# Optimization experiments

Hardware: AMD Instinct MI355X
Metric: run time of the kernel (lower is better)

Reference implementation:

```python
import jax, jax.numpy as jnp
import numpy as np
from jax import lax

N = 200000
CIN = 64
COUT = 128
K = 27  # 3^3 kernel offsets
EPS = 1e-5


def _make_rulebook(key, n, k):
    ki, km = jax.random.split(key)
    idx = jax.random.randint(ki, (k, n), 0, n, dtype=jnp.int32)
    keep = jax.random.uniform(km, (k, n)) < 0.5
    idx = jnp.where(keep, idx, -1)
    # center offset is always the voxel itself (submanifold conv)
    idx = idx.at[k // 2].set(jnp.arange(n, dtype=jnp.int32))
    return idx


def setup_inputs() -> dict:
    key = jax.random.key(0)
    ks = jax.random.split(key, 8)
    feats = jax.random.normal(ks[0], (N, CIN), dtype=jnp.float32)
    nbr1 = _make_rulebook(ks[1], N, K)
    nbr2 = _make_rulebook(ks[2], N, K)
    W1 = jax.random.normal(ks[3], (K, CIN, COUT), dtype=jnp.float32) * 0.05
    W2 = jax.random.normal(ks[4], (K, COUT, COUT), dtype=jnp.float32) * 0.05
    Wd = jax.random.normal(ks[5], (CIN, COUT), dtype=jnp.float32) * 0.05
    g1 = jnp.ones((COUT,), jnp.float32); b1 = jnp.zeros((COUT,), jnp.float32)
    g2 = jnp.ones((COUT,), jnp.float32); b2 = jnp.zeros((COUT,), jnp.float32)
    gd = jnp.ones((COUT,), jnp.float32); bd = jnp.zeros((COUT,), jnp.float32)
    return dict(feats=feats, nbr1=nbr1, nbr2=nbr2, W1=W1, W2=W2, Wd=Wd,
                g1=g1, b1=b1, g2=g2, b2=b2, gd=gd, bd=bd)


def sparse_conv(feats, W, nbr):
    """Rulebook sparse conv: gather neighbors per offset, GEMM, accumulate.
    feats: [N, Cin]; W: [K, Cin, Cout]; nbr: [K, N] int (-1 = missing)."""
    n = feats.shape[0]
    acc0 = jnp.zeros((n, W.shape[-1]), feats.dtype)

    def body(acc, xs):
        idx, Wk = xs  # [N], [Cin, Cout]
        valid = (idx >= 0).astype(feats.dtype)[:, None]
        g = feats[jnp.clip(idx, 0)] * valid  # masked gather [N, Cin]
        return acc + g @ Wk, None

    out, _ = lax.scan(body, acc0, (nbr, W))
    return out


def batchnorm(x, gamma, beta):
    mean = jnp.mean(x, axis=0)
    var = jnp.var(x, axis=0)
    return (x - mean) * lax.rsqrt(var + EPS) * gamma + beta


def reference(feats, nbr1, nbr2, W1, W2, Wd, g1, b1, g2, b2, gd, bd):
    h = sparse_conv(feats, W1, nbr1)
    h = jax.nn.relu(batchnorm(h, g1, b1))
    h = sparse_conv(h, W2, nbr2)
    h = batchnorm(h, g2, b2)
    skip = batchnorm(feats @ Wd, gd, bd)  # 1x1 conv downsample (Cin != Cout)
    return jax.nn.relu(h + skip)
```

## Files before the change

kernel.cpp:

```cpp
#include <hip/hip_runtime.h>
#include <stdint.h>

#define KOFF 27
#define CIN 64
#define COUT 128
#define EPS 1e-5f

using frag_ab = __attribute__((ext_vector_type(8))) short;
using frag_cd = __attribute__((ext_vector_type(4))) float;

__device__ __forceinline__ float bf2f(unsigned short u) {
  union { unsigned int i; float f; } x; x.i = ((unsigned int)u) << 16; return x.f;
}
__device__ __forceinline__ unsigned short f2bf(float f) {
  union { float f; unsigned int i; } x; x.f = f;
  unsigned int u = x.i;
  u += 0x7fffu + ((u >> 16) & 1u);
  return (unsigned short)(u >> 16);
}

__device__ __forceinline__ void gld16(const void* gptr, void* lptr) {
  __builtin_amdgcn_global_load_lds(
      (const __attribute__((address_space(1))) unsigned int*)gptr,
      (__attribute__((address_space(3))) unsigned int*)lptr, 16, 0, 0);
}

template <int CI, bool GATHER, bool OF32>
__global__ __launch_bounds__(256, 3) void conv_kernel(
    const unsigned short* __restrict__ X, const int* __restrict__ nbr,
    const unsigned short* __restrict__ Wt, void* __restrict__ Yv,
    const unsigned short* __restrict__ zpage, float* __restrict__ sums,
    int n, int koff) {
  constexpr int NC = CI / 32;
  __shared__ unsigned short Alds[3][128 * 32];
  __shared__ unsigned short Blds[3][128 * 32];

  const int tid = threadIdx.x;
  const int lane = tid & 63;
  const int wave = tid >> 6;
  const int row0 = blockIdx.x * 128;
  const int wrow = (wave >> 1) * 64;
  const int wcol = (wave & 1) * 64;
  const int m = lane & 15;
  const int q = lane >> 4;
  const int srow0 = wave * 16 + (lane >> 2);
  const int sl = lane & 3;

  frag_cd acc[4][4];
#pragma unroll
  for (int i = 0; i < 4; ++i)
#pragma unroll
    for (int j = 0; j < 4; ++j) acc[i][j] = (frag_cd){0.f, 0.f, 0.f, 0.f};

  int idxc[2], idxn[2];
  auto load_idx = [&](int ko, int (&dst)[2]) {
#pragma unroll
    for (int i = 0; i < 2; ++i) {
      const int grow = row0 + srow0 + i * 64;
      int v = -1;
      if (grow < n) v = GATHER ? nbr[(size_t)ko * n + grow] : grow;
      dst[i] = v;
    }
  };
  auto stage = [&](int buf, int ko, int kc, const int (&idx)[2]) {
#pragma unroll
    for (int i = 0; i < 2; ++i) {
      const int row = srow0 + i * 64;
      const int g = sl ^ ((row >> 1) & 3);
      const unsigned short* ga =
          (idx[i] >= 0) ? X + (size_t)idx[i] * CI + kc * 32 + g * 8 : zpage;
      gld16(ga, &Alds[buf][(i * 64 + wave * 16) * 32]);
      const unsigned short* gb =
          Wt + (size_t)ko * (128 * CI) + (size_t)row * CI + kc * 32 + g * 8;
      gld16(gb, &Blds[buf][(i * 64 + wave * 16) * 32]);
    }
  };
  auto do_mfma = [&](int buf) {
    frag_ab a[4], b[4];
#pragma unroll
    for (int i = 0; i < 4; ++i) {
      const int row = wrow + 16 * i + m;
      a[i] = *(const frag_ab*)(&Alds[buf][row * 32 + (q ^ ((row >> 1) & 3)) * 8]);
    }
#pragma unroll
    for (int j = 0; j < 4; ++j) {
      const int row = wcol + 16 * j + m;
      b[j] = *(const frag_ab*)(&Blds[buf][row * 32 + (q ^ ((row >> 1) & 3)) * 8]);
    }
#pragma unroll
    for (int i = 0; i < 4; ++i)
#pragma unroll
      for (int j = 0; j < 4; ++j)
        acc[i][j] = __builtin_amdgcn_mfma_f32_16x16x32_bf16(a[i], b[j],
                                                            acc[i][j], 0, 0, 0);
  };

  const int T = koff * NC;
  load_idx(0, idxc);
  stage(0, 0, 0, idxc);
  stage(1, 0, 1, idxc);
  if (koff > 1) load_idx(1, idxn);

  int bufc = 0;
  for (int t = 0; t < T - 1; ++t) {
    asm volatile("s_waitcnt vmcnt(4)" ::: "memory");
    __builtin_amdgcn_s_barrier();
    const int s = t + 2;
    if (s < T) {
      const int kos = s / NC;
      const int kcs = s & (NC - 1);
      if (kcs == 0) {
        idxc[0] = idxn[0];
        idxc[1] = idxn[1];
        if (kos + 1 < koff) load_idx(kos + 1, idxn);
      }
      int bufs = bufc + 2; if (bufs >= 3) bufs -= 3;
      stage(bufs, kos, kcs, idxc);
    }
    do_mfma(bufc);
    if (++bufc == 3) bufc = 0;
  }
  asm volatile("s_waitcnt vmcnt(0)" ::: "memory");
  __builtin_amdgcn_s_barrier();
  do_mfma(bufc);

#pragma unroll
  for (int j = 0; j < 4; ++j) {
    float s = 0.f, qq = 0.f;
#pragma unroll
    for (int i = 0; i < 4; ++i)
#pragma unroll
      for (int r = 0; r < 4; ++r) {
        float v = acc[i][j][r];
        s += v; qq += v * v;
      }
    s += __shfl_xor(s, 16); s += __shfl_xor(s, 32);
    qq += __shfl_xor(qq, 16); qq += __shfl_xor(qq, 32);
    if (lane < 16) {
      const int col = wcol + 16 * j + lane;
      atomicAdd(&sums[col], s);
      atomicAdd(&sums[COUT + col], qq);
    }
  }

#pragma unroll
  for (int i = 0; i < 4; ++i) {
#pragma unroll
    for (int r = 0; r < 4; ++r) {
      const int grow = row0 + wrow + 16 * i + q * 4 + r;
      if (grow < n) {
#pragma unroll
        for (int j = 0; j < 4; ++j) {
          const int gcol = wcol + 16 * j + m;
          if (OF32)
            ((float*)Yv)[(size_t)grow * COUT + gcol] = acc[i][j][r];
          else
            ((unsigned short*)Yv)[(size_t)grow * COUT + gcol] = f2bf(acc[i][j][r]);
        }
      }
    }
  }
}

__global__ void convert_kernel(const float* __restrict__ src,
                               unsigned short* __restrict__ dst, int total8) {
  int gid = blockIdx.x * 256 + threadIdx.x;
  if (gid >= total8) return;
  const float* s = src + (size_t)gid * 8;
  float4 lo = *(const float4*)s;
  float4 hi = *(const float4*)(s + 4);
  uint4 r;
  r.x = (unsigned)f2bf(lo.x) | ((unsigned)f2bf(lo.y) << 16);
  r.y = (unsigned)f2bf(lo.z) | ((unsigned)f2bf(lo.w) << 16);
  r.z = (unsigned)f2bf(hi.x) | ((unsigned)f2bf(hi.y) << 16);
  r.w = (unsigned)f2bf(hi.z) | ((unsigned)f2bf(hi.w) << 16);
  *(uint4*)(dst + (size_t)gid * 8) = r;
}

__global__ void transpose_w(const float* __restrict__ src,
                            unsigned short* __restrict__ dst, int kk, int ci,
                            int co) {
  int gid = blockIdx.x * blockDim.x + threadIdx.x;
  int total = kk * ci * co;
  if (gid >= total) return;
  int per = ci * co;
  int k = gid / per;
  int rem = gid - k * per;
  int o = rem / ci;
  int i = rem - o * ci;
  dst[gid] = f2bf(src[(size_t)k * per + (size_t)i * co + o]);
}

__global__ void finalize_kernel(const float* __restrict__ sums,
                                const float* __restrict__ gamma,
                                const float* __restrict__ beta,
                                float* __restrict__ scale,
                                float* __restrict__ shift, int n) {
  int c = threadIdx.x;
  float inv_n = 1.f / (float)n;
  float mean = sums[c] * inv_n;
  float var = sums[COUT + c] * inv_n - mean * mean;
  float sc = gamma[c] * rsqrtf(var + EPS);
  scale[c] = sc;
  shift[c] = beta[c] - mean * sc;
}

__global__ void norm_relu_kernel(unsigned short* __restrict__ x,
                                 const float* __restrict__ scale,
                                 const float* __restrict__ shift, int total8) {
  int gid = blockIdx.x * 256 + threadIdx.x;
  if (gid >= total8) return;
  size_t i = (size_t)gid * 8;
  int c0 = (int)(i & 127);
  uint4 v = *(const uint4*)(x + i);
  unsigned int w[4] = {v.x, v.y, v.z, v.w};
  unsigned int wo[4];
#pragma unroll
  for (int e = 0; e < 4; ++e) {
    int c = c0 + 2 * e;
    float f0 = bf2f((unsigned short)(w[e] & 0xffffu));
    float f1 = bf2f((unsigned short)(w[e] >> 16));
    f0 = fmaxf(f0 * scale[c] + shift[c], 0.f);
    f1 = fmaxf(f1 * scale[c + 1] + shift[c + 1], 0.f);
    wo[e] = (unsigned int)f2bf(f0) | ((unsigned int)f2bf(f1) << 16);
  }
  *(uint4*)(x + i) = make_uint4(wo[0], wo[1], wo[2], wo[3]);
}

__global__ void final_kernel(float* __restrict__ h2,
                             const unsigned short* __restrict__ s,
                             const float* __restrict__ scale2,
                             const float* __restrict__ shift2,
                             const float* __restrict__ scaled,
                             const float* __restrict__ shiftd, int total4) {
  int gid = blockIdx.x * 256 + threadIdx.x;
  if (gid >= total4) return;
  size_t i = (size_t)gid * 4;
  int c = (int)(i & 127);
  float4 a = *(const float4*)(h2 + i);
  uint2 sv = *(const uint2*)(s + i);
  float b0 = bf2f((unsigned short)(sv.x & 0xffffu));
  float b1 = bf2f((unsigned short)(sv.x >> 16));
  float b2 = bf2f((unsigned short)(sv.y & 0xffffu));
  float b3 = bf2f((unsigned short)(sv.y >> 16));
  float4 o;
  o.x = fmaxf(a.x * scale2[c] + shift2[c] + b0 * scaled[c] + shiftd[c], 0.f);
  o.y = fmaxf(a.y * scale2[c + 1] + shift2[c + 1] + b1 * scaled[c + 1] + shiftd[c + 1], 0.f);
  o.z = fmaxf(a.z * scale2[c + 2] + shift2[c + 2] + b2 * scaled[c + 2] + shiftd[c + 2], 0.f);
  o.w = fmaxf(a.w * scale2[c + 3] + shift2[c + 3] + b3 * scaled[c + 3] + shiftd[c + 3], 0.f);
  *(float4*)(h2 + i) = o;
}

extern "C" void kernel_launch(void* const* d_in, const int* in_sizes, int n_in,
                              void* d_out, int out_size, void* d_ws,
                              size_t ws_size, hipStream_t stream) {
  (void)n_in; (void)out_size; (void)ws_size;
  const float* feats = (const float*)d_in[0];
  const int* nbr1 = (const int*)d_in[1];
  const int* nbr2 = (const int*)d_in[2];
  const float* W1 = (const float*)d_in[3];
  const float* W2 = (const float*)d_in[4];
  const float* Wd = (const float*)d_in[5];
  const float* g1 = (const float*)d_in[6];
  const float* b1 = (const float*)d_in[7];
  const float* g2 = (const float*)d_in[8];
  const float* b2 = (const float*)d_in[9];
  const float* gd = (const float*)d_in[10];
  const float* bd = (const float*)d_in[11];

  const int n = in_sizes[0] / CIN;

  char* ws = (char*)d_ws;
  unsigned short* Wt1 = (unsigned short*)(ws);
  unsigned short* Wt2 = (unsigned short*)(ws + 442368);
  unsigned short* Wdt = (unsigned short*)(ws + 1327104);
  unsigned short* h1 = (unsigned short*)(ws + 1343488);
  unsigned short* sX = (unsigned short*)(ws + 52543488);
  float* sums1 = (float*)(ws + 103743488);
  float* sums2 = sums1 + 2 * COUT;
  float* sumsd = sums1 + 4 * COUT;
  float* scale1 = sums1 + 6 * COUT;
  float* shift1 = scale1 + COUT;
  float* scale2 = scale1 + 2 * COUT;
  float* shift2 = scale1 + 3 * COUT;
  float* scaled = scale1 + 4 * COUT;
  float* shiftd = scale1 + 5 * COUT;
  unsigned short* zpage = (unsigned short*)(ws + 103743488 + 8192);

  float* h2 = (float*)d_out;
  unsigned short* featsb = (unsigned short*)((char*)d_out + 76800000);

  hipMemsetAsync(sums1, 0, 8192 + 256, stream);

  transpose_w<<<(KOFF * CIN * COUT + 255) / 256, 256, 0, stream>>>(W1, Wt1, KOFF, CIN, COUT);
  transpose_w<<<(KOFF * COUT * COUT + 255) / 256, 256, 0, stream>>>(W2, Wt2, KOFF, COUT, COUT);
  transpose_w<<<(CIN * COUT + 255) / 256, 256, 0, stream>>>(Wd, Wdt, 1, CIN, COUT);

  const int f8 = n * CIN / 8;
  convert_kernel<<<(f8 + 255) / 256, 256, 0, stream>>>(feats, featsb, f8);

  const int mblocks = (n + 127) / 128;
  conv_kernel<CIN, true, false><<<mblocks, 256, 0, stream>>>(featsb, nbr1, Wt1, h1, zpage, sums1, n, KOFF);
  conv_kernel<CIN, false, false><<<mblocks, 256, 0, stream>>>(featsb, nullptr, Wdt, sX, zpage, sumsd, n, 1);

  finalize_kernel<<<1, COUT, 0, stream>>>(sums1, g1, b1, scale1, shift1, n);

  const int total8 = n * COUT / 8;
  norm_relu_kernel<<<(total8 + 255) / 256, 256, 0, stream>>>(h1, scale1, shift1, total8);

  conv_kernel<COUT, true, true><<<mblocks, 256, 0, stream>>>(h1, nbr2, Wt2, h2, zpage, sums2, n, KOFF);

  finalize_kernel<<<1, COUT, 0, stream>>>(sums2, g2, b2, scale2, shift2, n);
  finalize_kernel<<<1, COUT, 0, stream>>>(sumsd, gd, bd, scaled, shiftd, n);

  const int total4 = n * COUT / 4;
  final_kernel<<<(total4 + 255) / 256, 256, 0, stream>>>(h2, sX, scale2, shift2, scaled, shiftd, total4);
}
```

Measured before the change: 794.3 us.

## Load weight fragments directly into registers instead of staging through LDS

Removes the B (weight) LDS buffers and has each wave read its MFMA B fragments straight from global memory into registers, double-buffered one step ahead. The weights are pre-permuted into a fragment-friendly layout so each lane does contiguous 16-byte loads. This halves LDS usage and LDS read traffic per step, which may raise occupancy, but puts the weight loads on the L2/global path with register double-buffering and a retuned vmcnt wait.

```diff
diff --git a/kernel.cpp b/kernel.cpp
--- a/kernel.cpp
+++ b/kernel.cpp
@@ -33,7 +33,6 @@
     int n, int koff) {
   constexpr int NC = CI / 32;
   __shared__ unsigned short Alds[3][128 * 32];
-  __shared__ unsigned short Blds[3][128 * 32];
 
   const int tid = threadIdx.x;
   const int lane = tid & 63;
@@ -52,7 +51,9 @@
 #pragma unroll
     for (int j = 0; j < 4; ++j) acc[i][j] = (frag_cd){0.f, 0.f, 0.f, 0.f};
 
+  frag_ab bA[4], bB[4];
   int idxc[2], idxn[2];
+
   auto load_idx = [&](int ko, int (&dst)[2]) {
 #pragma unroll
     for (int i = 0; i < 2; ++i) {
@@ -62,7 +63,7 @@
       dst[i] = v;
     }
   };
-  auto stage = [&](int buf, int ko, int kc, const int (&idx)[2]) {
+  auto stageA = [&](int buf, int ko, int kc, const int (&idx)[2]) {
 #pragma unroll
     for (int i = 0; i < 2; ++i) {
       const int row = srow0 + i * 64;
@@ -70,24 +71,23 @@
       const unsigned short* ga =
           (idx[i] >= 0) ? X + (size_t)idx[i] * CI + kc * 32 + g * 8 : zpage;
       gld16(ga, &Alds[buf][(i * 64 + wave * 16) * 32]);
-      const unsigned short* gb =
-          Wt + (size_t)ko * (128 * CI) + (size_t)row * CI + kc * 32 + g * 8;
-      gld16(gb, &Blds[buf][(i * 64 + wave * 16) * 32]);
-    }
-  };
-  auto do_mfma = [&](int buf) {
-    frag_ab a[4], b[4];
+    }
+  };
+  auto loadB = [&](frag_ab (&b)[4], int ko, int kc) {
+    const unsigned short* base =
+        Wt + (size_t)(ko * NC + kc) * 4096 + q * 1024 + m * 8;
+#pragma unroll
+    for (int j = 0; j < 4; ++j)
+      b[j] = *(const frag_ab*)(base + (wcol + 16 * j) * 8);
+  };
+  auto do_mfma = [&](int buf, frag_ab (&b)[4]) {
+    frag_ab a[4];
 #pragma unroll
     for (int i = 0; i < 4; ++i) {
       const int row = wrow + 16 * i + m;
       a[i] = *(const frag_ab*)(&Alds[buf][row * 32 + (q ^ ((row >> 1) & 3)) * 8]);
     }
 #pragma unroll
-    for (int j = 0; j < 4; ++j) {
-      const int row = wcol + 16 * j + m;
-      b[j] = *(const frag_ab*)(&Blds[buf][row * 32 + (q ^ ((row >> 1) & 3)) * 8]);
-    }
-#pragma unroll
     for (int i = 0; i < 4; ++i)
 #pragma unroll
       for (int j = 0; j < 4; ++j)
@@ -97,32 +97,42 @@
 
   const int T = koff * NC;
   load_idx(0, idxc);
-  stage(0, 0, 0, idxc);
-  stage(1, 0, 1, idxc);
   if (koff > 1) load_idx(1, idxn);
+  stageA(0, 0, 0, idxc);
+  stageA(1, 0, 1, idxc);
+  loadB(bA, 0, 0);
 
   int bufc = 0;
-  for (int t = 0; t < T - 1; ++t) {
-    asm volatile("s_waitcnt vmcnt(4)" ::: "memory");
+  auto body = [&](int t, frag_ab (&bcur)[4], frag_ab (&bnxt)[4]) {
+    asm volatile("s_waitcnt vmcnt(6)" ::: "memory");
     __builtin_amdgcn_s_barrier();
     const int s = t + 2;
-    if (s < T) {
+    if (s < T && GATHER) {
       const int kos = s / NC;
-      const int kcs = s & (NC - 1);
-      if (kcs == 0) {
+      if ((s & (NC - 1)) == 0) {
         idxc[0] = idxn[0];
         idxc[1] = idxn[1];
         if (kos + 1 < koff) load_idx(kos + 1, idxn);
       }
+    }
+    const int u = t + 1;
+    if (u < T) loadB(bnxt, u / NC, u & (NC - 1));
+    if (s < T) {
       int bufs = bufc + 2; if (bufs >= 3) bufs -= 3;
-      stage(bufs, kos, kcs, idxc);
-    }
-    do_mfma(bufc);
+      stageA(bufs, s / NC, s & (NC - 1), idxc);
+    }
+    do_mfma(bufc, bcur);
     if (++bufc == 3) bufc = 0;
+  };
+
+  for (int t = 0; t + 3 < T; t += 2) {
+    body(t, bA, bB);
+    body(t + 1, bB, bA);
   }
+  body(T - 2, bA, bB);
   asm volatile("s_waitcnt vmcnt(0)" ::: "memory");
   __builtin_amdgcn_s_barrier();
-  do_mfma(bufc);
+  do_mfma(bufc, bB);
 
 #pragma unroll
   for (int j = 0; j < 4; ++j) {
@@ -178,17 +188,20 @@
 }
 
 __global__ void transpose_w(const float* __restrict__ src,
-                            unsigned short* __restrict__ dst, int kk, int ci,
-                            int co) {
+                            unsigned short* __restrict__ dst, int koff,
+                            int ci) {
   int gid = blockIdx.x * blockDim.x + threadIdx.x;
-  int total = kk * ci * co;
+  int total = koff * ci * 128;
   if (gid >= total) return;
-  int per = ci * co;
-  int k = gid / per;
-  int rem = gid - k * per;
-  int o = rem / ci;
-  int i = rem - o * ci;
-  dst[gid] = f2bf(src[(size_t)k * per + (size_t)i * co + o]);
+  int e = gid & 7;
+  int co = (gid >> 3) & 127;
+  int qq = (gid >> 10) & 3;
+  int slab = gid >> 12;
+  int nc = ci >> 5;
+  int ko = slab / nc;
+  int kc = slab - ko * nc;
+  int cin = kc * 32 + qq * 8 + e;
+  dst[gid] = f2bf(src[((size_t)ko * ci + cin) * 128 + co]);
 }
 
 __global__ void finalize_kernel(const float* __restrict__ sums,
@@ -292,9 +305,9 @@
 
   hipMemsetAsync(sums1, 0, 8192 + 256, stream);
 
-  transpose_w<<<(KOFF * CIN * COUT + 255) / 256, 256, 0, stream>>>(W1, Wt1, KOFF, CIN, COUT);
-  transpose_w<<<(KOFF * COUT * COUT + 255) / 256, 256, 0, stream>>>(W2, Wt2, KOFF, COUT, COUT);
-  transpose_w<<<(CIN * COUT + 255) / 256, 256, 0, stream>>>(Wd, Wdt, 1, CIN, COUT);
+  transpose_w<<<(KOFF * CIN * COUT + 255) / 256, 256, 0, stream>>>(W1, Wt1, KOFF, CIN);
+  transpose_w<<<(KOFF * COUT * COUT + 255) / 256, 256, 0, stream>>>(W2, Wt2, KOFF, COUT);
+  transpose_w<<<(CIN * COUT + 255) / 256, 256, 0, stream>>>(Wd, Wdt, 1, CIN);
 
   const int f8 = n * CIN / 8;
   convert_kernel<<<(f8 + 255) / 256, 256, 0, stream>>>(feats, featsb, f8);
```

Measured after the change: 696.0 us. 12.4% less time.
